# Kernel tuning notes

Measured on AMD Instinct MI355X. Metric: run time of the kernel, lower is better.

Reference implementation:

```python
import jax, jax.numpy as jnp
import numpy as np

D_MODEL = 1024
N_HEADS = 16
WINDOW = 256
CAUSAL = True


def build_sliding_window_mask(T, window_size, causal=True):
    half = window_size // 2
    i = jnp.arange(T)[:, None]
    j = jnp.arange(T)[None, :]
    attend = jnp.abs(i - j) <= half
    if causal:
        attend = attend & (j <= i)
    return jnp.where(attend, 0.0, -jnp.inf).astype(jnp.float32)  # (T, T)


def setup_inputs() -> dict:
    key = jax.random.key(0)
    kx, kq, kk, kv, ko = jax.random.split(key, 5)
    B, T, D = 2, 2048, D_MODEL
    s = 1.0 / np.sqrt(D)
    return {
        "x": jax.random.normal(kx, (B, T, D), jnp.float32),
        "Wq": jax.random.normal(kq, (D, D), jnp.float32) * s,
        "Wk": jax.random.normal(kk, (D, D), jnp.float32) * s,
        "Wv": jax.random.normal(kv, (D, D), jnp.float32) * s,
        "Wo": jax.random.normal(ko, (D, D), jnp.float32) * s,
    }


def reference(x, Wq, Wk, Wv, Wo):
    B, T, D = x.shape
    H = N_HEADS
    dh = D // H
    # torch nn.Linear: y = x @ W.T
    def proj(W):
        return (x @ W.T).reshape(B, T, H, dh).transpose(0, 2, 1, 3)  # (B,H,T,dh)

    q, k, v = proj(Wq), proj(Wk), proj(Wv)
    scale = jnp.sqrt(jnp.asarray(dh, x.dtype))
    scores = jnp.einsum("bhtd,bhsd->bhts", q, k) / scale  # (B,H,T,T)
    mask = build_sliding_window_mask(T, WINDOW, CAUSAL)
    scores = scores + mask[None, None]
    attn = jax.nn.softmax(scores, axis=-1)
    attn = jnp.nan_to_num(attn, nan=0.0)
    out = jnp.einsum("bhts,bhsd->bhtd", attn, v)  # (B,H,T,dh)
    out = out.transpose(0, 2, 1, 3).reshape(B, T, D)
    return out @ Wo.T
```

## Files before the change

### kernel.cpp

```cpp
#include <hip/hip_runtime.h>
#include <hip/hip_bf16.h>

#define B_  2
#define T_  2048
#define D_  1024
#define H_  16
#define DH_ 64
#define M_  (B_ * T_)

typedef short s16x8 __attribute__((ext_vector_type(8)));
typedef float f32x4 __attribute__((ext_vector_type(4)));

__device__ inline float bfu(unsigned short u) {
    union { unsigned int i; float f; } c; c.i = ((unsigned int)u) << 16; return c.f;
}
__device__ inline unsigned short f2bf(float f) {
    union { float f; unsigned int i; } c; c.f = f;
    unsigned int r = c.i + 0x7fffu + ((c.i >> 16) & 1u);
    return (unsigned short)(r >> 16);
}
__device__ inline void stv(float* p, float v) { *p = v; }
__device__ inline void stv(unsigned short* p, float v) { *p = f2bf(v); }

__device__ inline void gload_lds16(const unsigned short* g, unsigned short* l) {
    __builtin_amdgcn_global_load_lds(
        (const __attribute__((address_space(1))) void*)g,
        (__attribute__((address_space(3))) void*)l, 16, 0, 0);
}

__global__ __launch_bounds__(256) void conv_bf16(const float* __restrict__ x,
                                                 const float* __restrict__ Wq,
                                                 const float* __restrict__ Wk,
                                                 const float* __restrict__ Wv,
                                                 const float* __restrict__ Wo,
                                                 unsigned short* __restrict__ dst) {
    const int g = blockIdx.x * 256 + threadIdx.x;
    const float* s; size_t o;
    if (g < (1 << 20)) { s = x; o = (size_t)g; }
    else {
        int gg = g - (1 << 20);
        int w = gg >> 18;
        o = (size_t)(gg & ((1 << 18) - 1));
        s = (w == 0) ? Wq : (w == 1) ? Wk : (w == 2) ? Wv : Wo;
    }
    float4 v = ((const float4*)s)[o];
    ushort4 u;
    u.x = f2bf(v.x); u.y = f2bf(v.y); u.z = f2bf(v.z); u.w = f2bf(v.w);
    ((ushort4*)dst)[g] = u;
}

template <int BM, int NH, typename Tout>
__global__ __launch_bounds__(256) void gemm_m97(const unsigned short* __restrict__ A,
                                                const unsigned short* __restrict__ Bw,
                                                Tout* __restrict__ C0,
                                                Tout* __restrict__ C1,
                                                unsigned short* __restrict__ vtr,
                                                int K) {
    constexpr int MI = BM / 32;
    __shared__ unsigned short As[NH * BM * 32];
    __shared__ unsigned short Bs[NH * 128 * 32];
    const int tid  = threadIdx.x;
    const int lane = tid & 63;
    const int wave = tid >> 6;
    const int wr = wave >> 1, wc = wave & 1;
    const int bm = blockIdx.y * BM, bn = blockIdx.x * 128;
    const int fr = lane & 15, kg = lane >> 4;
    const int lrow = lane >> 2;
    const int lcol = (lane & 3) * 8;

    f32x4 acc[MI][4];
    #pragma unroll
    for (int mi = 0; mi < MI; ++mi)
        #pragma unroll
        for (int ni = 0; ni < 4; ++ni)
            #pragma unroll
            for (int r = 0; r < 4; ++r) acc[mi][ni][r] = 0.f;

    const unsigned short* ga = A  + (size_t)(bm + wave * 16 + lrow) * K + lcol;
    const unsigned short* gb = Bw + (size_t)(bn + wave * 16 + lrow) * K + lcol;
    unsigned short* la = &As[(wave * 16) * 32];
    unsigned short* lb = &Bs[(wave * 16) * 32];

    for (int k0 = 0; k0 < K; k0 += 32 * NH) {
        __syncthreads();
        #pragma unroll
        for (int hf = 0; hf < NH; ++hf) {
            #pragma unroll
            for (int s = 0; s < BM / 64; ++s)
                gload_lds16(ga + k0 + hf * 32 + (size_t)(s * 64) * K,
                            la + hf * BM * 32 + s * 64 * 32);
            gload_lds16(gb + k0 + hf * 32,                  lb + hf * 128 * 32);
            gload_lds16(gb + k0 + hf * 32 + (size_t)64 * K, lb + hf * 128 * 32 + 64 * 32);
        }
        __syncthreads();
        #pragma unroll
        for (int hf = 0; hf < NH; ++hf) {
            s16x8 af[MI], bfv[4];
            #pragma unroll
            for (int mi = 0; mi < MI; ++mi)
                af[mi] = *(const s16x8*)&As[hf * BM * 32 + (wr * (BM / 2) + mi * 16 + fr) * 32 + kg * 8];
            #pragma unroll
            for (int ni = 0; ni < 4; ++ni)
                bfv[ni] = *(const s16x8*)&Bs[hf * 128 * 32 + (wc * 64 + ni * 16 + fr) * 32 + kg * 8];
            #pragma unroll
            for (int mi = 0; mi < MI; ++mi)
                #pragma unroll
                for (int ni = 0; ni < 4; ++ni)
                    acc[mi][ni] = __builtin_amdgcn_mfma_f32_16x16x32_bf16(af[mi], bfv[ni], acc[mi][ni], 0, 0, 0);
        }
    }

    if (vtr && bn >= 2048) {
        #pragma unroll
        for (int mi = 0; mi < MI; ++mi)
            #pragma unroll
            for (int ni = 0; ni < 4; ++ni) {
                const int nl = (bn - 2048) + wc * 64 + ni * 16 + fr;
                const int h = nl >> 6, d = nl & 63;
                const int m0 = bm + wr * (BM / 2) + mi * 16 + kg * 4;
                const int b = m0 >> 11, t0 = m0 & (T_ - 1);
                ushort4 u;
                u.x = f2bf(acc[mi][ni][0]); u.y = f2bf(acc[mi][ni][1]);
                u.z = f2bf(acc[mi][ni][2]); u.w = f2bf(acc[mi][ni][3]);
                *(ushort4*)(vtr + ((size_t)(b * H_ + h) * 64 + d) * T_ + t0) = u;
            }
        return;
    }
    Tout* C = (bn < 1024) ? C0 : C1;
    const int nb = bn & 1023;
    #pragma unroll
    for (int mi = 0; mi < MI; ++mi)
        #pragma unroll
        for (int ni = 0; ni < 4; ++ni)
            #pragma unroll
            for (int r = 0; r < 4; ++r) {
                int m = bm + wr * (BM / 2) + mi * 16 + kg * 4 + r;
                int n = nb + wc * 64 + ni * 16 + fr;
                stv(&C[(size_t)m * 1024 + n], acc[mi][ni][r]);
            }
}

__global__ __launch_bounds__(256) void swa_mfma3(const unsigned short* qb,
                                                 const unsigned short* __restrict__ kb,
                                                 const unsigned short* __restrict__ vt,
                                                 unsigned short* ob) {
    __shared__ unsigned short Ks[192 * 64];
    __shared__ unsigned short Vs[64 * 208];
    __shared__ unsigned short Pl[4][16 * 168];
    const int wave = threadIdx.x >> 6;
    const int lane = threadIdx.x & 63;
    const int blk = blockIdx.x;
    const int i0b = (blk & 31) * 64;
    const int bh  = blk >> 5;
    const int h = bh & (H_ - 1), b = bh >> 4;
    const int g = lane >> 4, l15 = lane & 15;

    const size_t rowbase = (size_t)b * T_ * D_ + (size_t)h * DH_;
    const int klo2 = (i0b > 128) ? (i0b - 128) : 0;

    {
        const int lr = lane >> 3;
        const int gc = (lane & 7) ^ lr;
        const unsigned short* kg0 = kb + rowbase + (size_t)(klo2 + lr) * D_ + gc * 8;
        #pragma unroll
        for (int s = 0; s < 6; ++s) {
            const int i = wave * 6 + s;
            gload_lds16(kg0 + (size_t)(i * 8) * D_, &Ks[i * 8 * 64]);
        }
    }
    {
        const unsigned short* vtb = vt + (size_t)bh * 64 * T_ + klo2;
        #pragma unroll
        for (int s = 0; s < 7; ++s) {
            const int i = s * 4 + wave;
            if (i < 26) {
                const int cc = i * 64 + lane;
                const int d  = cc / 26;
                const int sl = cc - d * 26;
                const int c  = (sl < 24) ? (sl ^ (d & 7)) : sl;
                gload_lds16(vtb + (size_t)d * T_ + c * 8, &Vs[i * 512]);
            }
        }
    }

    const int i0  = i0b + wave * 16;
    const int klo = (i0 > 128) ? (i0 - 128) : 0;
    const int koff = klo - klo2;

    unsigned short* Pw = Pl[wave];
    {
        int row = lane >> 2, col = 144 + (lane & 3) * 4;
        *(uint2*)&Pw[row * 168 + col] = make_uint2(0u, 0u);
    }

    const unsigned short* qrow = qb + rowbase + (size_t)(i0 + l15) * D_ + g * 8;
    const s16x8 aq0 = *(const s16x8*)(qrow);
    const s16x8 aq1 = *(const s16x8*)(qrow + 32);

    __syncthreads();

    f32x4 sacc[9];
    #pragma unroll
    for (int t = 0; t < 9; ++t)
        #pragma unroll
        for (int r = 0; r < 4; ++r) sacc[t][r] = 0.f;

    #pragma unroll
    for (int t = 0; t < 9; ++t) {
        const int row = koff + t * 16 + l15;
        const int r7 = row & 7;
        s16x8 b0 = *(const s16x8*)&Ks[row * 64 + ((g     ^ r7) * 8)];
        s16x8 b1 = *(const s16x8*)&Ks[row * 64 + (((g+4) ^ r7) * 8)];
        sacc[t] = __builtin_amdgcn_mfma_f32_16x16x32_bf16(aq0, b0, sacc[t], 0, 0, 0);
        sacc[t] = __builtin_amdgcn_mfma_f32_16x16x32_bf16(aq1, b1, sacc[t], 0, 0, 0);
    }

    float mrow[4] = {-1e30f, -1e30f, -1e30f, -1e30f};
    #pragma unroll
    for (int t = 0; t < 9; ++t)
        #pragma unroll
        for (int r = 0; r < 4; ++r) {
            const int j  = klo + t * 16 + l15;
            const int iq = i0 + g * 4 + r;
            const bool valid = (j <= iq) && (j + 128 >= iq);
            const float s = valid ? sacc[t][r] * 0.125f : -1e30f;
            sacc[t][r] = s;
            mrow[r] = fmaxf(mrow[r], s);
        }
    #pragma unroll
    for (int r = 0; r < 4; ++r)
        #pragma unroll
        for (int off = 1; off < 16; off <<= 1)
            mrow[r] = fmaxf(mrow[r], __shfl_xor(mrow[r], off));

    float lrow[4] = {0.f, 0.f, 0.f, 0.f};
    #pragma unroll
    for (int t = 0; t < 9; ++t)
        #pragma unroll
        for (int r = 0; r < 4; ++r) {
            const float p = __expf(sacc[t][r] - mrow[r]);
            sacc[t][r] = p;
            lrow[r] += p;
        }
    #pragma unroll
    for (int r = 0; r < 4; ++r) {
        #pragma unroll
        for (int off = 1; off < 16; off <<= 1)
            lrow[r] += __shfl_xor(lrow[r], off);
    }
    float invl[4];
    #pragma unroll
    for (int r = 0; r < 4; ++r) invl[r] = 1.f / lrow[r];

    #pragma unroll
    for (int t = 0; t < 9; ++t)
        #pragma unroll
        for (int r = 0; r < 4; ++r)
            Pw[(g * 4 + r) * 168 + t * 16 + l15] = f2bf(sacc[t][r]);

    f32x4 oacc[4];
    #pragma unroll
    for (int nt = 0; nt < 4; ++nt)
        #pragma unroll
        for (int r = 0; r < 4; ++r) oacc[nt][r] = 0.f;

    const int kc0 = koff >> 3;
    #pragma unroll
    for (int kt = 0; kt < 5; ++kt) {
        const s16x8 ap = *(const s16x8*)&Pw[l15 * 168 + kt * 32 + g * 8];
        #pragma unroll
        for (int nt = 0; nt < 4; ++nt) {
            const int d = nt * 16 + l15;
            const int c = kc0 + kt * 4 + g;
            const int sl = (c < 24) ? (c ^ (d & 7)) : c;
            s16x8 bv = *(const s16x8*)&Vs[d * 208 + sl * 8];
            oacc[nt] = __builtin_amdgcn_mfma_f32_16x16x32_bf16(ap, bv, oacc[nt], 0, 0, 0);
        }
    }

    #pragma unroll
    for (int nt = 0; nt < 4; ++nt)
        #pragma unroll
        for (int r = 0; r < 4; ++r) {
            const float val = oacc[nt][r] * invl[r];
            ob[rowbase + (size_t)(i0 + g * 4 + r) * D_ + nt * 16 + l15] = f2bf(val);
        }
}

extern "C" void kernel_launch(void* const* d_in, const int* in_sizes, int n_in,
                              void* d_out, int out_size, void* d_ws, size_t ws_size,
                              hipStream_t stream) {
    const float* x  = (const float*)d_in[0];
    const float* Wq = (const float*)d_in[1];
    const float* Wk = (const float*)d_in[2];
    const float* Wv = (const float*)d_in[3];
    const float* Wo = (const float*)d_in[4];

    const size_t MD = (size_t)M_ * D_;
    const size_t WN = (size_t)D_ * D_;

    unsigned short* wsb = (unsigned short*)d_ws;
    unsigned short* xb  = wsb;
    unsigned short* Wqb = xb + MD;
    unsigned short* Wob = Wqb + 3 * WN;
    unsigned short* qb  = Wob + WN;
    unsigned short* vt = (unsigned short*)d_out;
    unsigned short* kb = vt + MD;

    conv_bf16<<<8192, 256, 0, stream>>>(x, Wq, Wk, Wv, Wo, wsb);

    gemm_m97<128, 2, unsigned short><<<dim3(24, M_ / 128), 256, 0, stream>>>(
        xb, Wqb, qb, kb, vt, D_);

    swa_mfma3<<<(B_ * H_ * T_) / 64, 256, 0, stream>>>(qb, kb, vt, qb);

    gemm_m97<64, 4, float><<<dim3(8, M_ / 64), 256, 0, stream>>>(
        qb, Wob, (float*)d_out, (float*)d_out, nullptr, D_);
}
```

Measured before the change: 149.4 us.

## Halve GEMM N-tile to 64 and alias attention P buffer onto K tile LDS

The GEMM kernel gets a BN template parameter. Both the QKV projection and the output projection now use 64-wide N tiles, which doubles the number of blocks in each grid. This is meant to improve occupancy and load balance across CUs, at the cost of more A-tile reloads. The attention kernel drops its separate per-wave P scratch in LDS and reuses the K tile region after a new barrier, lowering LDS use per block so more blocks can be resident. The price is one extra __syncthreads after the QK^T step.

```diff
diff --git a/kernel.cpp b/kernel.cpp
--- a/kernel.cpp
+++ b/kernel.cpp
@@ -49,7 +49,7 @@
     ((ushort4*)dst)[g] = u;
 }
 
-template <int BM, int NH, typename Tout>
+template <int BM, int BN, int NH, typename Tout>
 __global__ __launch_bounds__(256) void gemm_m97(const unsigned short* __restrict__ A,
                                                 const unsigned short* __restrict__ Bw,
                                                 Tout* __restrict__ C0,
@@ -57,22 +57,23 @@
                                                 unsigned short* __restrict__ vtr,
                                                 int K) {
     constexpr int MI = BM / 32;
+    constexpr int NI = BN / 32;
     __shared__ unsigned short As[NH * BM * 32];
-    __shared__ unsigned short Bs[NH * 128 * 32];
+    __shared__ unsigned short Bs[NH * BN * 32];
     const int tid  = threadIdx.x;
     const int lane = tid & 63;
     const int wave = tid >> 6;
     const int wr = wave >> 1, wc = wave & 1;
-    const int bm = blockIdx.y * BM, bn = blockIdx.x * 128;
+    const int bm = blockIdx.y * BM, bn = blockIdx.x * BN;
     const int fr = lane & 15, kg = lane >> 4;
     const int lrow = lane >> 2;
     const int lcol = (lane & 3) * 8;
 
-    f32x4 acc[MI][4];
+    f32x4 acc[MI][NI];
     #pragma unroll
     for (int mi = 0; mi < MI; ++mi)
         #pragma unroll
-        for (int ni = 0; ni < 4; ++ni)
+        for (int ni = 0; ni < NI; ++ni)
             #pragma unroll
             for (int r = 0; r < 4; ++r) acc[mi][ni][r] = 0.f;
 
@@ -89,23 +90,25 @@
             for (int s = 0; s < BM / 64; ++s)
                 gload_lds16(ga + k0 + hf * 32 + (size_t)(s * 64) * K,
                             la + hf * BM * 32 + s * 64 * 32);
-            gload_lds16(gb + k0 + hf * 32,                  lb + hf * 128 * 32);
-            gload_lds16(gb + k0 + hf * 32 + (size_t)64 * K, lb + hf * 128 * 32 + 64 * 32);
+            #pragma unroll
+            for (int s = 0; s < BN / 64; ++s)
+                gload_lds16(gb + k0 + hf * 32 + (size_t)(s * 64) * K,
+                            lb + hf * BN * 32 + s * 64 * 32);
         }
         __syncthreads();
         #pragma unroll
         for (int hf = 0; hf < NH; ++hf) {
-            s16x8 af[MI], bfv[4];
+            s16x8 af[MI], bfv[NI];
             #pragma unroll
             for (int mi = 0; mi < MI; ++mi)
                 af[mi] = *(const s16x8*)&As[hf * BM * 32 + (wr * (BM / 2) + mi * 16 + fr) * 32 + kg * 8];
             #pragma unroll
-            for (int ni = 0; ni < 4; ++ni)
-                bfv[ni] = *(const s16x8*)&Bs[hf * 128 * 32 + (wc * 64 + ni * 16 + fr) * 32 + kg * 8];
+            for (int ni = 0; ni < NI; ++ni)
+                bfv[ni] = *(const s16x8*)&Bs[hf * BN * 32 + (wc * (BN / 2) + ni * 16 + fr) * 32 + kg * 8];
             #pragma unroll
             for (int mi = 0; mi < MI; ++mi)
                 #pragma unroll
-                for (int ni = 0; ni < 4; ++ni)
+                for (int ni = 0; ni < NI; ++ni)
                     acc[mi][ni] = __builtin_amdgcn_mfma_f32_16x16x32_bf16(af[mi], bfv[ni], acc[mi][ni], 0, 0, 0);
         }
     }
@@ -114,8 +117,8 @@
         #pragma unroll
         for (int mi = 0; mi < MI; ++mi)
             #pragma unroll
-            for (int ni = 0; ni < 4; ++ni) {
-                const int nl = (bn - 2048) + wc * 64 + ni * 16 + fr;
+            for (int ni = 0; ni < NI; ++ni) {
+                const int nl = (bn - 2048) + wc * (BN / 2) + ni * 16 + fr;
                 const int h = nl >> 6, d = nl & 63;
                 const int m0 = bm + wr * (BM / 2) + mi * 16 + kg * 4;
                 const int b = m0 >> 11, t0 = m0 & (T_ - 1);
@@ -131,22 +134,21 @@
     #pragma unroll
     for (int mi = 0; mi < MI; ++mi)
         #pragma unroll
-        for (int ni = 0; ni < 4; ++ni)
+        for (int ni = 0; ni < NI; ++ni)
             #pragma unroll
             for (int r = 0; r < 4; ++r) {
                 int m = bm + wr * (BM / 2) + mi * 16 + kg * 4 + r;
-                int n = nb + wc * 64 + ni * 16 + fr;
+                int n = nb + wc * (BN / 2) + ni * 16 + fr;
                 stv(&C[(size_t)m * 1024 + n], acc[mi][ni][r]);
             }
 }
 
-__global__ __launch_bounds__(256) void swa_mfma3(const unsigned short* qb,
+__global__ __launch_bounds__(256) void swa_mfma4(const unsigned short* qb,
                                                  const unsigned short* __restrict__ kb,
                                                  const unsigned short* __restrict__ vt,
                                                  unsigned short* ob) {
     __shared__ unsigned short Ks[192 * 64];
     __shared__ unsigned short Vs[64 * 208];
-    __shared__ unsigned short Pl[4][16 * 168];
     const int wave = threadIdx.x >> 6;
     const int lane = threadIdx.x & 63;
     const int blk = blockIdx.x;
@@ -187,12 +189,6 @@
     const int klo = (i0 > 128) ? (i0 - 128) : 0;
     const int koff = klo - klo2;
 
-    unsigned short* Pw = Pl[wave];
-    {
-        int row = lane >> 2, col = 144 + (lane & 3) * 4;
-        *(uint2*)&Pw[row * 168 + col] = make_uint2(0u, 0u);
-    }
-
     const unsigned short* qrow = qb + rowbase + (size_t)(i0 + l15) * D_ + g * 8;
     const s16x8 aq0 = *(const s16x8*)(qrow);
     const s16x8 aq1 = *(const s16x8*)(qrow + 32);
@@ -213,6 +209,13 @@
         s16x8 b1 = *(const s16x8*)&Ks[row * 64 + (((g+4) ^ r7) * 8)];
         sacc[t] = __builtin_amdgcn_mfma_f32_16x16x32_bf16(aq0, b0, sacc[t], 0, 0, 0);
         sacc[t] = __builtin_amdgcn_mfma_f32_16x16x32_bf16(aq1, b1, sacc[t], 0, 0, 0);
+    }
+
+    __syncthreads();
+    unsigned short* Pw = &Ks[wave * (16 * 168)];
+    {
+        int row = lane >> 2, col = 144 + (lane & 3) * 4;
+        *(uint2*)&Pw[row * 168 + col] = make_uint2(0u, 0u);
     }
 
     float mrow[4] = {-1e30f, -1e30f, -1e30f, -1e30f};
@@ -309,11 +312,11 @@
 
     conv_bf16<<<8192, 256, 0, stream>>>(x, Wq, Wk, Wv, Wo, wsb);
 
-    gemm_m97<128, 2, unsigned short><<<dim3(24, M_ / 128), 256, 0, stream>>>(
+    gemm_m97<128, 64, 2, unsigned short><<<dim3(48, M_ / 128), 256, 0, stream>>>(
         xb, Wqb, qb, kb, vt, D_);
 
-    swa_mfma3<<<(B_ * H_ * T_) / 64, 256, 0, stream>>>(qb, kb, vt, qb);
-
-    gemm_m97<64, 4, float><<<dim3(8, M_ / 64), 256, 0, stream>>>(
+    swa_mfma4<<<(B_ * H_ * T_) / 64, 256, 0, stream>>>(qb, kb, vt, qb);
+
+    gemm_m97<64, 64, 4, float><<<dim3(16, M_ / 64), 256, 0, stream>>>(
         qb, Wob, (float*)d_out, (float*)d_out, nullptr, D_);
 }
```

Result: slower. 157.9 us (+5.7%).
